# Performance work log

Measured on AMD Instinct MI355X. Metric: run time of the kernel, lower is better.

Reference implementation:

```python
import jax, jax.numpy as jnp
import numpy as np

N_NODES = 2048
N_FLUID = 400000
N_SOLID = 400000


def setup_inputs() -> dict:
    key = jax.random.key(0)
    k1, k2, k3 = jax.random.split(key, 3)
    nodes = jax.random.uniform(k1, (N_NODES, 3), dtype=jnp.float32)
    # sorted distinct node ids per tet: sort 4 draws from [0, N-4) then add offsets 0..3
    fe = jnp.sort(jax.random.randint(k2, (N_FLUID, 4), 0, N_NODES - 4), axis=1) + jnp.arange(4)
    se = jnp.sort(jax.random.randint(k3, (N_SOLID, 4), 0, N_NODES - 4), axis=1) + jnp.arange(4)
    return {
        "nodes": nodes,
        "fluid_elements": fe.astype(jnp.int32),
        "solid_elements": se.astype(jnp.int32),
        "E_mod": jnp.float32(2.1e11),
        "nu": jnp.float32(0.3),
        "rho_s": jnp.float32(7850.0),
    }


def _grads_and_volume(coords):
    """coords: [E,4,3] -> shape-fn gradients [E,4,3], volume [E]."""
    ones = jnp.ones(coords.shape[:-1] + (1,), coords.dtype)
    A = jnp.concatenate([ones, coords], axis=-1)
    A_inv = jnp.linalg.inv(A)
    grads = jnp.swapaxes(A_inv[..., 1:, :], -1, -2)        # [E,4,3]
    v0 = coords[:, 1] - coords[:, 0]
    v1 = coords[:, 2] - coords[:, 0]
    v2 = coords[:, 3] - coords[:, 0]
    vol = jnp.abs(jnp.linalg.det(jnp.stack([v0, v1, v2], axis=-1))) / 6.0  # [E]
    return grads, vol


def _fluid_element_matrices(coords):
    grads, vol = _grads_and_volume(coords)
    K_e = vol[:, None, None] * jnp.einsum("eik,ejk->eij", grads, grads)      # [E,4,4]
    m_template = (2.0 * jnp.eye(4, dtype=coords.dtype) + jnp.ones((4, 4), coords.dtype)) / 10.0
    M_e = vol[:, None, None] * m_template
    return K_e, M_e


def _elasticity_D(E_mod, nu):
    coeff = E_mod / ((1.0 + nu) * (1.0 - 2.0 * nu))
    top = nu * jnp.ones((3, 3), jnp.float32) + (1.0 - 2.0 * nu) * jnp.eye(3, dtype=jnp.float32)
    D = jnp.zeros((6, 6), jnp.float32)
    D = D.at[:3, :3].set(top)
    D = D.at[3:, 3:].set(((1.0 - 2.0 * nu) / 2.0) * jnp.eye(3, dtype=jnp.float32))
    return coeff * D


def _solid_element_matrices(coords, E_mod, nu, rho_s):
    grads, vol = _grads_and_volume(coords)                 # grads [E,4,3]
    bx, by, bz = grads[..., 0], grads[..., 1], grads[..., 2]   # each [E,4]
    z = jnp.zeros_like(bx)
    # per-node 6x3 strain-displacement block -> [E,4,6,3]
    block = jnp.stack([
        jnp.stack([bx, z, z], axis=-1),
        jnp.stack([z, by, z], axis=-1),
        jnp.stack([z, z, bz], axis=-1),
        jnp.stack([by, bx, z], axis=-1),
        jnp.stack([z, bz, by], axis=-1),
        jnp.stack([bz, z, bx], axis=-1),
    ], axis=-2)
    E = coords.shape[0]
    B = jnp.transpose(block, (0, 2, 1, 3)).reshape(E, 6, 12)  # [E,6,12]
    D = _elasticity_D(E_mod, nu)                              # [6,6]
    K_e = vol[:, None, None] * jnp.einsum("eai,ab,ebj->eij", B, D, B)  # [E,12,12]
    M_e = (rho_s * vol / 4.0)[:, None, None] * jnp.eye(12, dtype=coords.dtype)
    return K_e, M_e


def reference(nodes, fluid_elements, solid_elements, E_mod, nu, rho_s):
    n = nodes.shape[0]
    # ---- fluid: local matrices + scatter-add assembly into [N,N] ----
    cf = nodes[fluid_elements]                              # [Ef,4,3]
    Kf_e, Mf_e = _fluid_element_matrices(cf)
    rows = fluid_elements[:, :, None]                       # [Ef,4,1]
    cols = fluid_elements[:, None, :]                       # [Ef,1,4]
    K_f = jnp.zeros((n, n), jnp.float32).at[rows, cols].add(Kf_e)
    M_f = jnp.zeros((n, n), jnp.float32).at[rows, cols].add(Mf_e)
    # ---- solid: 3 dof/node, assembly into [3N,3N] ----
    cs = nodes[solid_elements]                              # [Es,4,3]
    Ks_e, Ms_e = _solid_element_matrices(cs, E_mod, nu, rho_s)
    dofs = (3 * solid_elements[:, :, None] + jnp.arange(3)).reshape(solid_elements.shape[0], 12)
    K_s = jnp.zeros((3 * n, 3 * n), jnp.float32).at[dofs[:, :, None], dofs[:, None, :]].add(Ks_e)
    M_s = jnp.zeros((3 * n, 3 * n), jnp.float32).at[dofs[:, :, None], dofs[:, None, :]].add(Ms_e)
    return (K_f, M_f, K_s, M_s)
```

## Files before the change

### kernel.cpp

```cpp
#include <hip/hip_runtime.h>


#define G_PART 256

__device__ __forceinline__ float sel4(float x0, float x1, float x2, float x3, int a) {
    float r = x0;
    r = (a == 1) ? x1 : r;
    r = (a == 2) ? x2 : r;
    r = (a == 3) ? x3 : r;
    return r;
}
__device__ __forceinline__ int sel4i(int x0, int x1, int x2, int x3, int a) {
    int r = x0;
    r = (a == 1) ? x1 : r;
    r = (a == 2) ? x2 : r;
    r = (a == 3) ? x3 : r;
    return r;
}

__device__ __forceinline__ float wave_reduce(float v) {
#pragma unroll
    for (int m = 1; m < 64; m <<= 1) v += __shfl_xor(v, m, 64);
    return v;
}

__device__ __forceinline__ void tet_geom_f(const float* __restrict__ nodes,
                                           int n0, int n1, int n2, int n3_,
                                           float& gx1, float& gy1, float& gz1,
                                           float& gx2, float& gy2, float& gz2,
                                           float& gx3, float& gy3, float& gz3,
                                           float& volf)
{
    const float* q0 = nodes + 3ll * n0;
    const float* q1 = nodes + 3ll * n1;
    const float* q2 = nodes + 3ll * n2;
    const float* q3 = nodes + 3ll * n3_;
    double p0x = q0[0], p0y = q0[1], p0z = q0[2];
    double r1x = (double)q1[0] - p0x, r1y = (double)q1[1] - p0y, r1z = (double)q1[2] - p0z;
    double r2x = (double)q2[0] - p0x, r2y = (double)q2[1] - p0y, r2z = (double)q2[2] - p0z;
    double r3x = (double)q3[0] - p0x, r3y = (double)q3[1] - p0y, r3z = (double)q3[2] - p0z;
    double c23x = r2y*r3z - r2z*r3y, c23y = r2z*r3x - r2x*r3z, c23z = r2x*r3y - r2y*r3x;
    double det = r1x*c23x + r1y*c23y + r1z*c23z;
    double inv = 1.0 / det;
    double c31x = r3y*r1z - r3z*r1y, c31y = r3z*r1x - r3x*r1z, c31z = r3x*r1y - r3y*r1x;
    double c12x = r1y*r2z - r1z*r2y, c12y = r1z*r2x - r1x*r2z, c12z = r1x*r2y - r1y*r2x;
    gx1 = (float)(c23x*inv); gy1 = (float)(c23y*inv); gz1 = (float)(c23z*inv);
    gx2 = (float)(c31x*inv); gy2 = (float)(c31y*inv); gz2 = (float)(c31z*inv);
    gx3 = (float)(c12x*inv); gy3 = (float)(c12y*inv); gz3 = (float)(c12z*inv);
    volf = (float)(fabs(det) / 6.0);
}

__device__ __forceinline__ int fetch_entry(const int* __restrict__ ent,
                                           const int* __restrict__ Sb,
                                           const int* __restrict__ Qb,
                                           int chunk4, int v)
{
    int lo = 0, hi = 255;
#pragma unroll
    for (int it = 0; it < 8; ++it) {
        int mid = (lo + hi + 1) >> 1;
        bool ge = (Qb[mid] <= v);
        lo = ge ? mid : lo;
        hi = ge ? hi : mid - 1;
    }
    return ent[(size_t)lo * chunk4 + Sb[lo] + (v - Qb[lo])];
}

#define DECL_VISIT(P) \
    float P##gx0=0,P##gx1=0,P##gx2=0,P##gx3=0, P##gy0=0,P##gy1=0,P##gy2=0,P##gy3=0, \
          P##gz0=0,P##gz1=0,P##gz2=0,P##gz3=0, P##vol=0, P##ga0=0,P##ga1=0,P##ga2=0; \
    int P##a=0, P##c0=0,P##c1=0,P##c2=0,P##c3=0;

#define LOAD_VISIT(P, packed_) do { \
    int e_ = (packed_) >> 2; P##a = (packed_) & 3; \
    int4 nd_ = elems4[e_]; \
    P##c0 = nd_.x; P##c1 = nd_.y; P##c2 = nd_.z; P##c3 = nd_.w; \
    tet_geom_f(nodes, nd_.x, nd_.y, nd_.z, nd_.w, \
        P##gx1,P##gy1,P##gz1, P##gx2,P##gy2,P##gz2, P##gx3,P##gy3,P##gz3, P##vol); \
    P##gx0 = -(P##gx1+P##gx2+P##gx3); \
    P##gy0 = -(P##gy1+P##gy2+P##gy3); \
    P##gz0 = -(P##gz1+P##gz2+P##gz3); \
    P##ga0 = sel4(P##gx0,P##gx1,P##gx2,P##gx3,P##a); \
    P##ga1 = sel4(P##gy0,P##gy1,P##gy2,P##gy3,P##a); \
    P##ga2 = sel4(P##gz0,P##gz1,P##gz2,P##gz3,P##a); \
} while (0)

#define DIAG_S(P) do { \
    float lv_ = lam*P##vol, mv_ = mu*P##vol, lm_ = lv_+mv_; \
    float mgg_ = mv_*(P##ga0*P##ga0 + P##ga1*P##ga1 + P##ga2*P##ga2); \
    d00 += lm_*P##ga0*P##ga0 + mgg_; d01 += lm_*P##ga0*P##ga1;        d02 += lm_*P##ga0*P##ga2; \
    d10 += lm_*P##ga1*P##ga0;        d11 += lm_*P##ga1*P##ga1 + mgg_; d12 += lm_*P##ga1*P##ga2; \
    d20 += lm_*P##ga2*P##ga0;        d21 += lm_*P##ga2*P##ga1;        d22 += lm_*P##ga2*P##ga2 + mgg_; \
    vsum += P##vol; } while (0)

#define DIAG_F(P) do { \
    dK += P##vol*(P##ga0*P##ga0 + P##ga1*P##ga1 + P##ga2*P##ga2); \
    dM += P##vol*0.3f; } while (0)

#define PAIR_S(P, b_) do { \
    float gb0_ = sel4(P##gx0,P##gx1,P##gx2,P##gx3,b_); \
    float gb1_ = sel4(P##gy0,P##gy1,P##gy2,P##gy3,b_); \
    float gb2_ = sel4(P##gz0,P##gz1,P##gz2,P##gz3,b_); \
    col = sel4i(P##c0,P##c1,P##c2,P##c3,b_); \
    float lv_ = lam*P##vol, mv_ = mu*P##vol; \
    float la0_ = lv_*P##ga0, la1_ = lv_*P##ga1, la2_ = lv_*P##ga2; \
    float ma0_ = mv_*P##ga0, ma1_ = mv_*P##ga1, ma2_ = mv_*P##ga2; \
    float mgg_ = mv_*(P##ga0*gb0_ + P##ga1*gb1_ + P##ga2*gb2_); \
    v00 = la0_*gb0_ + ma0_*gb0_ + mgg_; v01 = la0_*gb1_ + ma1_*gb0_; v02 = la0_*gb2_ + ma2_*gb0_; \
    v10 = la1_*gb0_ + ma0_*gb1_; v11 = la1_*gb1_ + ma1_*gb1_ + mgg_; v12 = la1_*gb2_ + ma2_*gb1_; \
    v20 = la2_*gb0_ + ma0_*gb2_; v21 = la2_*gb1_ + ma1_*gb2_; v22 = la2_*gb2_ + ma2_*gb2_ + mgg_; \
} while (0)

#define PAIR_F(P, b_) do { \
    float gb0_ = sel4(P##gx0,P##gx1,P##gx2,P##gx3,b_); \
    float gb1_ = sel4(P##gy0,P##gy1,P##gy2,P##gy3,b_); \
    float gb2_ = sel4(P##gz0,P##gz1,P##gz2,P##gz3,b_); \
    col = sel4i(P##c0,P##c1,P##c2,P##c3,b_); \
    vK = P##vol*(P##ga0*gb0_ + P##ga1*gb1_ + P##ga2*gb2_); \
    vM = P##vol*0.1f; \
} while (0)

__global__ void __launch_bounds__(256)
index_build(const int4* __restrict__ fe, const int4* __restrict__ se,
            int* __restrict__ entF, int* __restrict__ entS,
            int* __restrict__ PF, int* __restrict__ PS,
            int nf, int ns, int n, int chunkF, int chunkS)
{
    extern __shared__ int h[];
    int* wsum = h + n;
    const bool solid = blockIdx.x >= G_PART;
    const int b = solid ? blockIdx.x - G_PART : blockIdx.x;
    const int4* elems = solid ? se : fe;
    const int nelem = solid ? ns : nf;
    const int chunk = solid ? chunkS : chunkF;
    int* P = (solid ? PS : PF) + (size_t)b * (n + 1);
    int* entries = (solid ? entS : entF) + (size_t)b * 4 * chunk;

    const int t = threadIdx.x;
    const int beg = b * chunk, end = min(nelem, beg + chunk);

    for (int i = t; i < n; i += 256) h[i] = 0;
    __syncthreads();
    for (int e = beg + t; e < end; e += 256) {
        int4 nd = elems[e];
        atomicAdd(&h[nd.x], 1);
        atomicAdd(&h[nd.y], 1);
        atomicAdd(&h[nd.z], 1);
        atomicAdd(&h[nd.w], 1);
    }
    __syncthreads();

    const int cs = (n + 255) / 256;
    const int base = t * cs;
    int s = 0;
    for (int k = 0; k < cs; ++k) {
        int i = base + k;
        if (i < n) s += h[i];
    }
    wsum[t] = s;
    __syncthreads();
    for (int d = 1; d < 256; d <<= 1) {
        int v = (t >= d) ? wsum[t - d] : 0;
        __syncthreads();
        wsum[t] += v;
        __syncthreads();
    }
    int run = (t == 0) ? 0 : wsum[t - 1];
    for (int k = 0; k < cs; ++k) {
        int i = base + k;
        if (i < n) { int c = h[i]; h[i] = run; P[i] = run; run += c; }
    }
    if (t == 255) P[n] = wsum[255];
    __syncthreads();

    for (int e = beg + t; e < end; e += 256) {
        int4 nd = elems[e];
        int p;
        p = atomicAdd(&h[nd.x], 1); entries[p] = e * 4 + 0;
        p = atomicAdd(&h[nd.y], 1); entries[p] = e * 4 + 1;
        p = atomicAdd(&h[nd.z], 1); entries[p] = e * 4 + 2;
        p = atomicAdd(&h[nd.w], 1); entries[p] = e * 4 + 3;
    }
}

__global__ void __launch_bounds__(512, 4)
fused_gather(const int* __restrict__ entF, const int* __restrict__ PF,
             const int* __restrict__ entS, const int* __restrict__ PS,
             const int4* __restrict__ fe, const int4* __restrict__ se,
             const float* __restrict__ nodes,
             float* __restrict__ Kf, float* __restrict__ Mf,
             float* __restrict__ Ks, float* __restrict__ Ms,
             const float* __restrict__ E_p, const float* __restrict__ nu_p,
             const float* __restrict__ rho_p, int n, int n3,
             int chunk4F, int chunk4S)
{
    extern __shared__ unsigned char smem[];
    const int tid = threadIdx.x;
    const int bid = blockIdx.x;

    if (bid < n) {
        const int r = bid;
        const int4* elems4 = se;
        float* val = (float*)smem;
        unsigned short* claim = (unsigned short*)(val + 9 * n);
        int* Sb = (int*)(claim + n);
        int* Qb = Sb + 256;
        float* dred = (float*)(Qb + 257);

        {
            float4* v = (float4*)val;
            int cnt = (9 * n) >> 2;
            for (int k = tid; k < cnt; k += 512) v[k] = make_float4(0.f,0.f,0.f,0.f);
        }
        if (tid < 256) {
            const int* Pp = PS + (size_t)tid * (n + 1) + r;
            int s0 = Pp[0], e0 = Pp[1];
            Sb[tid] = s0;
            Qb[tid] = e0 - s0;
        }
        __syncthreads();
        if (tid < 64) {
            int c0 = Qb[4*tid], c1 = Qb[4*tid+1], c2 = Qb[4*tid+2], c3 = Qb[4*tid+3];
            int s = c0 + c1 + c2 + c3;
            int x = s;
#pragma unroll
            for (int d = 1; d < 64; d <<= 1) {
                int y = __shfl_up(x, d, 64);
                if (tid >= d) x += y;
            }
            int ex = x - s;
            Qb[4*tid] = ex; Qb[4*tid+1] = ex + c0;
            Qb[4*tid+2] = ex + c0 + c1; Qb[4*tid+3] = ex + c0 + c1 + c2;
            if (tid == 63) Qb[256] = ex + s;
        }
        __syncthreads();
        const int T = Qb[256];

        float E = *E_p, nu = *nu_p, rho = *rho_p;
        float coeff = E / ((1.f + nu) * (1.f - 2.f * nu));
        float lam = coeff * nu;
        float mu  = coeff * (1.f - 2.f * nu) * 0.5f;

        float d00=0,d01=0,d02=0,d10=0,d11=0,d12=0,d20=0,d21=0,d22=0,vsum=0;
        DECL_VISIT(A_);
        DECL_VISIT(B_);

        bool pending = false, validB = false;
        int s, col = 0, nextV = tid + 1024;
        float v00=0,v01=0,v02=0,v10=0,v11=0,v12=0,v20=0,v21=0,v22=0;

        const int vi0 = tid, vi1 = tid + 512;
        if (vi0 < T) {
            int pk = fetch_entry(entS, Sb, Qb, chunk4S, vi0);
            LOAD_VISIT(A_, pk); DIAG_S(A_); s = 0;
        } else s = 6;
        if (vi1 < T) {
            int pk = fetch_entry(entS, Sb, Qb, chunk4S, vi1);
            LOAD_VISIT(B_, pk); DIAG_S(B_); validB = true;
        }

        auto advanceS = [&]() {
            while (!pending) {
                if (s >= 6 || (s >= 3 && !validB)) {
                    if (nextV >= T) return;
                    int pk = fetch_entry(entS, Sb, Qb, chunk4S, nextV);
                    LOAD_VISIT(B_, pk); DIAG_S(B_);
                    validB = true; nextV += 512; s = 3;
                }
                if (s < 3) { int t_ = s;     int b_ = t_ + (t_ >= A_a ? 1 : 0); PAIR_S(A_, b_); }
                else       { int t_ = s - 3; int b_ = t_ + (t_ >= B_a ? 1 : 0); PAIR_S(B_, b_); }
                ++s; pending = true;
            }
        };

        advanceS();
        int live = __syncthreads_count(pending ? 1 : 0);
        while (live) {
            if (pending) claim[col] = (unsigned short)tid;
            __syncthreads();
            if (pending && claim[col] == (unsigned short)tid) {
                float* p0 = val + 3 * col;
                float* p1 = p0 + n3;
                float* p2 = p1 + n3;
                p0[0]+=v00; p0[1]+=v01; p0[2]+=v02;
                p1[0]+=v10; p1[1]+=v11; p1[2]+=v12;
                p2[0]+=v20; p2[1]+=v21; p2[2]+=v22;
                pending = false;
                advanceS();
            }
            live = __syncthreads_count(pending ? 1 : 0);
        }

        d00=wave_reduce(d00); d01=wave_reduce(d01); d02=wave_reduce(d02);
        d10=wave_reduce(d10); d11=wave_reduce(d11); d12=wave_reduce(d12);
        d20=wave_reduce(d20); d21=wave_reduce(d21); d22=wave_reduce(d22);
        vsum=wave_reduce(vsum);
        if ((tid & 63) == 0) {
            int w = tid >> 6;
            dred[w*10+0]=d00; dred[w*10+1]=d01; dred[w*10+2]=d02;
            dred[w*10+3]=d10; dred[w*10+4]=d11; dred[w*10+5]=d12;
            dred[w*10+6]=d20; dred[w*10+7]=d21; dred[w*10+8]=d22;
            dred[w*10+9]=vsum;
        }
        __syncthreads();
        if (tid < 10) {
            float t_ = 0.f;
            for (int w = 0; w < 8; ++w) t_ += dred[w*10 + tid];
            dred[80 + tid] = t_;
        }
        __syncthreads();
        if (tid < 9) {
            int i = tid / 3, j = tid - 3 * i;
            val[i * n3 + 3 * r + j] += dred[80 + tid];
        }
        __syncthreads();

        int q = n3 >> 2;
        for (int k4 = tid; k4 < 3 * q; k4 += 512) {
            int i = (k4 >= q) + (k4 >= 2*q);
            int t4 = k4 - i * q;
            float4 w = ((const float4*)(val + i * n3))[t4];
            ((float4*)(Ks + (size_t)(3*r + i) * n3))[t4] = w;
        }
        float diag = rho * 0.25f * dred[89];
        for (int k4 = tid; k4 < 3 * q; k4 += 512) {
            int i = (k4 >= q) + (k4 >= 2*q);
            int t4 = k4 - i * q;
            int dcol = 3*r + i;
            int base = t4 << 2;
            float4 w;
            w.x = (base + 0 == dcol) ? diag : 0.f;
            w.y = (base + 1 == dcol) ? diag : 0.f;
            w.z = (base + 2 == dcol) ? diag : 0.f;
            w.w = (base + 3 == dcol) ? diag : 0.f;
            ((float4*)(Ms + (size_t)(3*r + i) * n3))[t4] = w;
        }
    } else {
        const int r = bid - n;
        const int4* elems4 = fe;
        float* val = (float*)smem;
        unsigned short* claim = (unsigned short*)(val + 2 * n);
        int* Sb = (int*)(claim + n);
        int* Qb = Sb + 256;
        float* dred = (float*)(Qb + 257);

        {
            float4* v = (float4*)val;
            int cnt = (2 * n) >> 2;
            for (int k = tid; k < cnt; k += 512) v[k] = make_float4(0.f,0.f,0.f,0.f);
        }
        if (tid < 256) {
            const int* Pp = PF + (size_t)tid * (n + 1) + r;
            int s0 = Pp[0], e0 = Pp[1];
            Sb[tid] = s0;
            Qb[tid] = e0 - s0;
        }
        __syncthreads();
        if (tid < 64) {
            int c0 = Qb[4*tid], c1 = Qb[4*tid+1], c2 = Qb[4*tid+2], c3 = Qb[4*tid+3];
            int s = c0 + c1 + c2 + c3;
            int x = s;
#pragma unroll
            for (int d = 1; d < 64; d <<= 1) {
                int y = __shfl_up(x, d, 64);
                if (tid >= d) x += y;
            }
            int ex = x - s;
            Qb[4*tid] = ex; Qb[4*tid+1] = ex + c0;
            Qb[4*tid+2] = ex + c0 + c1; Qb[4*tid+3] = ex + c0 + c1 + c2;
            if (tid == 63) Qb[256] = ex + s;
        }
        __syncthreads();
        const int T = Qb[256];

        float dK = 0.f, dM = 0.f;
        DECL_VISIT(A_);
        DECL_VISIT(B_);

        bool pending = false, validB = false;
        int s, col = 0, nextV = tid + 1024;
        float vK = 0.f, vM = 0.f;

        const int vi0 = tid, vi1 = tid + 512;
        if (vi0 < T) {
            int pk = fetch_entry(entF, Sb, Qb, chunk4F, vi0);
            LOAD_VISIT(A_, pk); DIAG_F(A_); s = 0;
        } else s = 6;
        if (vi1 < T) {
            int pk = fetch_entry(entF, Sb, Qb, chunk4F, vi1);
            LOAD_VISIT(B_, pk); DIAG_F(B_); validB = true;
        }

        auto advanceF = [&]() {
            while (!pending) {
                if (s >= 6 || (s >= 3 && !validB)) {
                    if (nextV >= T) return;
                    int pk = fetch_entry(entF, Sb, Qb, chunk4F, nextV);
                    LOAD_VISIT(B_, pk); DIAG_F(B_);
                    validB = true; nextV += 512; s = 3;
                }
                if (s < 3) { int t_ = s;     int b_ = t_ + (t_ >= A_a ? 1 : 0); PAIR_F(A_, b_); }
                else       { int t_ = s - 3; int b_ = t_ + (t_ >= B_a ? 1 : 0); PAIR_F(B_, b_); }
                ++s; pending = true;
            }
        };

        advanceF();
        int live = __syncthreads_count(pending ? 1 : 0);
        while (live) {
            if (pending) claim[col] = (unsigned short)tid;
            __syncthreads();
            if (pending && claim[col] == (unsigned short)tid) {
                val[col]     += vK;
                val[n + col] += vM;
                pending = false;
                advanceF();
            }
            live = __syncthreads_count(pending ? 1 : 0);
        }

        dK = wave_reduce(dK);
        dM = wave_reduce(dM);
        if ((tid & 63) == 0) { int w = tid >> 6; dred[w*2+0] = dK; dred[w*2+1] = dM; }
        __syncthreads();
        if (tid < 2) {
            float t_ = 0.f;
            for (int w = 0; w < 8; ++w) t_ += dred[w*2 + tid];
            dred[16 + tid] = t_;
        }
        __syncthreads();
        if (tid == 0) { val[r] += dred[16]; val[n + r] += dred[17]; }
        __syncthreads();

        size_t rowoff = (size_t)r * n;
        int qf = n >> 2;
        float4* K4 = (float4*)(Kf + rowoff);
        float4* M4 = (float4*)(Mf + rowoff);
        for (int c4 = tid; c4 < qf; c4 += 512) {
            K4[c4] = ((const float4*)val)[c4];
            M4[c4] = ((const float4*)(val + n))[c4];
        }
    }
}

__device__ __forceinline__ void tet_grads_d(const float* __restrict__ nodes,
                                            const int* ni, double g[4][3], double& vol)
{
    double p[4][3];
#pragma unroll
    for (int a = 0; a < 4; ++a) {
        const float* q = nodes + 3ll * ni[a];
        p[a][0] = (double)q[0]; p[a][1] = (double)q[1]; p[a][2] = (double)q[2];
    }
    double r1[3], r2[3], r3[3];
#pragma unroll
    for (int k = 0; k < 3; ++k) {
        r1[k] = p[1][k] - p[0][k];
        r2[k] = p[2][k] - p[0][k];
        r3[k] = p[3][k] - p[0][k];
    }
    double c23[3] = { r2[1]*r3[2]-r2[2]*r3[1], r2[2]*r3[0]-r2[0]*r3[2], r2[0]*r3[1]-r2[1]*r3[0] };
    double det = r1[0]*c23[0] + r1[1]*c23[1] + r1[2]*c23[2];
    double inv = 1.0 / det;
    double c31[3] = { r3[1]*r1[2]-r3[2]*r1[1], r3[2]*r1[0]-r3[0]*r1[2], r3[0]*r1[1]-r3[1]*r1[0] };
    double c12[3] = { r1[1]*r2[2]-r1[2]*r2[1], r1[2]*r2[0]-r1[0]*r2[2], r1[0]*r2[1]-r1[1]*r2[0] };
#pragma unroll
    for (int k = 0; k < 3; ++k) {
        g[1][k] = c23[k]*inv; g[2][k] = c31[k]*inv; g[3][k] = c12[k]*inv;
        g[0][k] = -(g[1][k] + g[2][k] + g[3][k]);
    }
    vol = fabs(det) / 6.0;
}

__global__ void __launch_bounds__(256)
fluid_assemble(const float* __restrict__ nodes, const int* __restrict__ elems,
               float* __restrict__ Kf, float* __restrict__ Mf, int nelem, int n)
{
    int e = blockIdx.x * blockDim.x + threadIdx.x;
    if (e >= nelem) return;
    const int4 nd = *reinterpret_cast<const int4*>(elems + 4ll * e);
    int ni[4] = { nd.x, nd.y, nd.z, nd.w };
    double g[4][3], vol;
    tet_grads_d(nodes, ni, g, vol);
#pragma unroll
    for (int a = 0; a < 4; ++a) {
        long long rowoff = (long long)ni[a] * n;
#pragma unroll
        for (int b = 0; b < 4; ++b) {
            double kv = vol * (g[a][0]*g[b][0] + g[a][1]*g[b][1] + g[a][2]*g[b][2]);
            double mv = vol * (a == b ? 0.3 : 0.1);
            atomicAdd(Kf + rowoff + ni[b], (float)kv);
            atomicAdd(Mf + rowoff + ni[b], (float)mv);
        }
    }
}

__global__ void __launch_bounds__(256)
solid_assemble(const float* __restrict__ nodes, const int* __restrict__ elems,
               float* __restrict__ Ks, float* __restrict__ Ms,
               const float* __restrict__ E_p, const float* __restrict__ nu_p,
               const float* __restrict__ rho_p, int nelem, int n3)
{
    int e = blockIdx.x * blockDim.x + threadIdx.x;
    if (e >= nelem) return;
    double E = (double)*E_p, nu = (double)*nu_p, rho = (double)*rho_p;
    double coeff = E / ((1.0 + nu) * (1.0 - 2.0 * nu));
    double lam = coeff * nu, mu = coeff * (1.0 - 2.0 * nu) * 0.5;
    const int4 nd = *reinterpret_cast<const int4*>(elems + 4ll * e);
    int ni[4] = { nd.x, nd.y, nd.z, nd.w };
    double g[4][3], vol;
    tet_grads_d(nodes, ni, g, vol);
    double lv = lam * vol, mv = mu * vol;
#pragma unroll
    for (int a = 0; a < 4; ++a) {
        long long row0 = 3ll * ni[a];
#pragma unroll
        for (int b = 0; b < 4; ++b) {
            long long col0 = 3ll * ni[b];
            double gg = g[a][0]*g[b][0] + g[a][1]*g[b][1] + g[a][2]*g[b][2];
#pragma unroll
            for (int i = 0; i < 3; ++i) {
                float* rowp = Ks + (row0 + i) * (long long)n3 + col0;
#pragma unroll
                for (int j = 0; j < 3; ++j) {
                    double val = lv * g[a][i] * g[b][j] + mv * g[a][j] * g[b][i];
                    if (i == j) val += mv * gg;
                    atomicAdd(rowp + j, (float)val);
                }
            }
        }
        float mval = (float)(rho * vol * 0.25);
#pragma unroll
        for (int i = 0; i < 3; ++i) {
            long long d = row0 + i;
            atomicAdd(Ms + d * (long long)n3 + d, mval);
        }
    }
}

extern "C" void kernel_launch(void* const* d_in, const int* in_sizes, int n_in,
                              void* d_out, int out_size, void* d_ws, size_t ws_size,
                              hipStream_t stream)
{
    const float* nodes = (const float*)d_in[0];
    const int*   fe    = (const int*)d_in[1];
    const int*   se    = (const int*)d_in[2];
    const float* E_p   = (const float*)d_in[3];
    const float* nu_p  = (const float*)d_in[4];
    const float* rho_p = (const float*)d_in[5];

    const int n  = in_sizes[0] / 3;
    const int nf = in_sizes[1] / 4;
    const int ns = in_sizes[2] / 4;
    const int n3 = 3 * n;

    float* out = (float*)d_out;
    float* Kf = out;
    float* Mf = Kf + (size_t)n * n;
    float* Ks = Mf + (size_t)n * n;
    float* Ms = Ks + (size_t)n3 * n3;

    const int chunkF = (nf + G_PART - 1) / G_PART;
    const int chunkS = (ns + G_PART - 1) / G_PART;

    size_t pos = 0;
    auto take = [&](size_t bytes) {
        size_t p = pos;
        pos = (pos + bytes + 255) & ~(size_t)255;
        return p;
    };
    size_t entF_o = take((size_t)4 * chunkF * G_PART * 4);
    size_t entS_o = take((size_t)4 * chunkS * G_PART * 4);
    size_t PF_o   = take((size_t)G_PART * (n + 1) * 4);
    size_t PS_o   = take((size_t)G_PART * (n + 1) * 4);

    size_t gatherLds = (size_t)9 * n * 4 + (size_t)n * 2 + (256 + 257) * 4 + 96 * 4;
    size_t indexLds  = (size_t)(n + 256) * 4;
    bool gather_ok = (pos <= ws_size) && ((n & 3) == 0) && (n <= 65535) &&
                     (gatherLds <= 160 * 1024) && (indexLds <= 64 * 1024);

    const int bs = 256;

    if (!gather_ok) {
        hipMemsetAsync(d_out, 0, (size_t)out_size * sizeof(float), stream);
        fluid_assemble<<<(nf + bs - 1) / bs, bs, 0, stream>>>(nodes, fe, Kf, Mf, nf, n);
        solid_assemble<<<(ns + bs - 1) / bs, bs, 0, stream>>>(nodes, se, Ks, Ms,
                                                              E_p, nu_p, rho_p, ns, n3);
        return;
    }

    char* ws = (char*)d_ws;
    int* entF = (int*)(ws + entF_o);
    int* entS = (int*)(ws + entS_o);
    int* PF   = (int*)(ws + PF_o);
    int* PS   = (int*)(ws + PS_o);

    const int4* fe4 = (const int4*)fe;
    const int4* se4 = (const int4*)se;

    index_build<<<2 * G_PART, bs, indexLds, stream>>>(fe4, se4, entF, entS, PF, PS,
                                                      nf, ns, n, chunkF, chunkS);
    fused_gather<<<2 * n, 512, gatherLds, stream>>>(entF, PF, entS, PS,
                                                    fe4, se4, nodes,
                                                    Kf, Mf, Ks, Ms,
                                                    E_p, nu_p, rho_p, n, n3,
                                                    4 * chunkF, 4 * chunkS);
}
```

Before: 199.6 us.

## Batch per-visit column claims into lock-step rounds and transpose partition offsets

Replaces the one-pending-write-per-thread claim loop with a round-based scheme. Each thread claims all three remaining columns of both loaded visits at once, then applies every claim it wins. This cuts the number of block-wide barriers per row. The partition prefix array is transposed so per-row offset loads are coalesced. The initial visits look up their partition through an LDS table instead of binary search. Fluid and solid blocks are interleaved by block index, and the LDS limit check is tightened, which changes occupancy and shifts more inputs to the fallback path.

```diff
diff --git a/kernel.cpp b/kernel.cpp
--- a/kernel.cpp
+++ b/kernel.cpp
@@ -50,10 +50,10 @@
     volf = (float)(fabs(det) / 6.0);
 }
 
-__device__ __forceinline__ int fetch_entry(const int* __restrict__ ent,
-                                           const int* __restrict__ Sb,
-                                           const int* __restrict__ Qb,
-                                           int chunk4, int v)
+__device__ __forceinline__ int fetch_entry_bs(const int* __restrict__ ent,
+                                              const int* __restrict__ Sb,
+                                              const int* __restrict__ Qb,
+                                              int chunk4, int v)
 {
     int lo = 0, hi = 255;
 #pragma unroll
@@ -69,12 +69,11 @@
 #define DECL_VISIT(P) \
     float P##gx0=0,P##gx1=0,P##gx2=0,P##gx3=0, P##gy0=0,P##gy1=0,P##gy2=0,P##gy3=0, \
           P##gz0=0,P##gz1=0,P##gz2=0,P##gz3=0, P##vol=0, P##ga0=0,P##ga1=0,P##ga2=0; \
-    int P##a=0, P##c0=0,P##c1=0,P##c2=0,P##c3=0;
+    int P##a=0, P##k0=0, P##k1=0, P##k2=0;
 
 #define LOAD_VISIT(P, packed_) do { \
     int e_ = (packed_) >> 2; P##a = (packed_) & 3; \
     int4 nd_ = elems4[e_]; \
-    P##c0 = nd_.x; P##c1 = nd_.y; P##c2 = nd_.z; P##c3 = nd_.w; \
     tet_geom_f(nodes, nd_.x, nd_.y, nd_.z, nd_.w, \
         P##gx1,P##gy1,P##gz1, P##gx2,P##gy2,P##gz2, P##gx3,P##gy3,P##gz3, P##vol); \
     P##gx0 = -(P##gx1+P##gx2+P##gx3); \
@@ -83,6 +82,9 @@
     P##ga0 = sel4(P##gx0,P##gx1,P##gx2,P##gx3,P##a); \
     P##ga1 = sel4(P##gy0,P##gy1,P##gy2,P##gy3,P##a); \
     P##ga2 = sel4(P##gz0,P##gz1,P##gz2,P##gz3,P##a); \
+    P##k0 = sel4i(nd_.x, nd_.y, nd_.z, nd_.w, 0 + ((0 >= P##a) ? 1 : 0)); \
+    P##k1 = sel4i(nd_.x, nd_.y, nd_.z, nd_.w, 1 + ((1 >= P##a) ? 1 : 0)); \
+    P##k2 = sel4i(nd_.x, nd_.y, nd_.z, nd_.w, 2 + ((2 >= P##a) ? 1 : 0)); \
 } while (0)
 
 #define DIAG_S(P) do { \
@@ -97,28 +99,39 @@
     dK += P##vol*(P##ga0*P##ga0 + P##ga1*P##ga1 + P##ga2*P##ga2); \
     dM += P##vol*0.3f; } while (0)
 
-#define PAIR_S(P, b_) do { \
-    float gb0_ = sel4(P##gx0,P##gx1,P##gx2,P##gx3,b_); \
-    float gb1_ = sel4(P##gy0,P##gy1,P##gy2,P##gy3,b_); \
-    float gb2_ = sel4(P##gz0,P##gz1,P##gz2,P##gz3,b_); \
-    col = sel4i(P##c0,P##c1,P##c2,P##c3,b_); \
-    float lv_ = lam*P##vol, mv_ = mu*P##vol; \
-    float la0_ = lv_*P##ga0, la1_ = lv_*P##ga1, la2_ = lv_*P##ga2; \
-    float ma0_ = mv_*P##ga0, ma1_ = mv_*P##ga1, ma2_ = mv_*P##ga2; \
-    float mgg_ = mv_*(P##ga0*gb0_ + P##ga1*gb1_ + P##ga2*gb2_); \
-    v00 = la0_*gb0_ + ma0_*gb0_ + mgg_; v01 = la0_*gb1_ + ma1_*gb0_; v02 = la0_*gb2_ + ma2_*gb0_; \
-    v10 = la1_*gb0_ + ma0_*gb1_; v11 = la1_*gb1_ + ma1_*gb1_ + mgg_; v12 = la1_*gb2_ + ma2_*gb1_; \
-    v20 = la2_*gb0_ + ma0_*gb2_; v21 = la2_*gb1_ + ma1_*gb2_; v22 = la2_*gb2_ + ma2_*gb2_ + mgg_; \
-} while (0)
-
-#define PAIR_F(P, b_) do { \
-    float gb0_ = sel4(P##gx0,P##gx1,P##gx2,P##gx3,b_); \
-    float gb1_ = sel4(P##gy0,P##gy1,P##gy2,P##gy3,b_); \
-    float gb2_ = sel4(P##gz0,P##gz1,P##gz2,P##gz3,b_); \
-    col = sel4i(P##c0,P##c1,P##c2,P##c3,b_); \
-    vK = P##vol*(P##ga0*gb0_ + P##ga1*gb1_ + P##ga2*gb2_); \
-    vM = P##vol*0.1f; \
-} while (0)
+#define WIN_S(P, K, BIT) \
+    if ((slots & (BIT)) && claim[P##k##K] == (unsigned short)tid) { \
+        int b_ = (K) + (((K) >= P##a) ? 1 : 0); \
+        float gb0_ = sel4(P##gx0,P##gx1,P##gx2,P##gx3,b_); \
+        float gb1_ = sel4(P##gy0,P##gy1,P##gy2,P##gy3,b_); \
+        float gb2_ = sel4(P##gz0,P##gz1,P##gz2,P##gz3,b_); \
+        float lv_ = lam*P##vol, mv_ = mu*P##vol; \
+        float la0_=lv_*P##ga0, la1_=lv_*P##ga1, la2_=lv_*P##ga2; \
+        float ma0_=mv_*P##ga0, ma1_=mv_*P##ga1, ma2_=mv_*P##ga2; \
+        float mgg_ = mv_*(P##ga0*gb0_ + P##ga1*gb1_ + P##ga2*gb2_); \
+        float* p0_ = val + 3*P##k##K; float* p1_ = p0_ + n3; float* p2_ = p1_ + n3; \
+        p0_[0] += la0_*gb0_ + ma0_*gb0_ + mgg_; \
+        p0_[1] += la0_*gb1_ + ma1_*gb0_; \
+        p0_[2] += la0_*gb2_ + ma2_*gb0_; \
+        p1_[0] += la1_*gb0_ + ma0_*gb1_; \
+        p1_[1] += la1_*gb1_ + ma1_*gb1_ + mgg_; \
+        p1_[2] += la1_*gb2_ + ma2_*gb1_; \
+        p2_[0] += la2_*gb0_ + ma0_*gb2_; \
+        p2_[1] += la2_*gb1_ + ma1_*gb2_; \
+        p2_[2] += la2_*gb2_ + ma2_*gb2_ + mgg_; \
+        slots &= ~(BIT); \
+    }
+
+#define WIN_F(P, K, BIT) \
+    if ((slots & (BIT)) && claim[P##k##K] == (unsigned short)tid) { \
+        int b_ = (K) + (((K) >= P##a) ? 1 : 0); \
+        float gb0_ = sel4(P##gx0,P##gx1,P##gx2,P##gx3,b_); \
+        float gb1_ = sel4(P##gy0,P##gy1,P##gy2,P##gy3,b_); \
+        float gb2_ = sel4(P##gz0,P##gz1,P##gz2,P##gz3,b_); \
+        val[P##k##K]     += P##vol*(P##ga0*gb0_ + P##ga1*gb1_ + P##ga2*gb2_); \
+        val[n + P##k##K] += P##vol*0.1f; \
+        slots &= ~(BIT); \
+    }
 
 __global__ void __launch_bounds__(256)
 index_build(const int4* __restrict__ fe, const int4* __restrict__ se,
@@ -133,7 +146,7 @@
     const int4* elems = solid ? se : fe;
     const int nelem = solid ? ns : nf;
     const int chunk = solid ? chunkS : chunkF;
-    int* P = (solid ? PS : PF) + (size_t)b * (n + 1);
+    int* P2 = solid ? PS : PF;
     int* entries = (solid ? entS : entF) + (size_t)b * 4 * chunk;
 
     const int t = threadIdx.x;
@@ -168,9 +181,13 @@
     int run = (t == 0) ? 0 : wsum[t - 1];
     for (int k = 0; k < cs; ++k) {
         int i = base + k;
-        if (i < n) { int c = h[i]; h[i] = run; P[i] = run; run += c; }
-    }
-    if (t == 255) P[n] = wsum[255];
+        if (i < n) {
+            int c = h[i]; h[i] = run;
+            P2[(size_t)i * G_PART + b] = run;
+            run += c;
+        }
+    }
+    if (t == 255) P2[(size_t)n * G_PART + b] = wsum[255];
     __syncthreads();
 
     for (int e = beg + t; e < end; e += 256) {
@@ -197,15 +214,17 @@
     extern __shared__ unsigned char smem[];
     const int tid = threadIdx.x;
     const int bid = blockIdx.x;
-
-    if (bid < n) {
-        const int r = bid;
+    const bool isSolid = (bid & 1) == 0;
+    const int r = bid >> 1;
+
+    if (isSolid) {
         const int4* elems4 = se;
         float* val = (float*)smem;
         unsigned short* claim = (unsigned short*)(val + 9 * n);
         int* Sb = (int*)(claim + n);
         int* Qb = Sb + 256;
         float* dred = (float*)(Qb + 257);
+        int* flg = (int*)(dred + 90);
 
         {
             float4* v = (float4*)val;
@@ -213,11 +232,12 @@
             for (int k = tid; k < cnt; k += 512) v[k] = make_float4(0.f,0.f,0.f,0.f);
         }
         if (tid < 256) {
-            const int* Pp = PS + (size_t)tid * (n + 1) + r;
-            int s0 = Pp[0], e0 = Pp[1];
+            int s0 = PS[(size_t)r * G_PART + tid];
+            int e0 = PS[(size_t)(r + 1) * G_PART + tid];
             Sb[tid] = s0;
             Qb[tid] = e0 - s0;
         }
+        if (tid == 0) { flg[0] = 0; flg[1] = 0; }
         __syncthreads();
         if (tid < 64) {
             int c0 = Qb[4*tid], c1 = Qb[4*tid+1], c2 = Qb[4*tid+2], c3 = Qb[4*tid+3];
@@ -235,6 +255,13 @@
         }
         __syncthreads();
         const int T = Qb[256];
+        const int pvLim = min(T, n);
+
+        if (tid < 256) {
+            int v0 = Qb[tid], v1 = min(Qb[tid + 1], pvLim);
+            for (int v = v0; v < v1; ++v) claim[v] = (unsigned short)tid;
+        }
+        __syncthreads();
 
         float E = *E_p, nu = *nu_p, rho = *rho_p;
         float coeff = E / ((1.f + nu) * (1.f - 2.f * nu));
@@ -245,50 +272,49 @@
         DECL_VISIT(A_);
         DECL_VISIT(B_);
 
-        bool pending = false, validB = false;
-        int s, col = 0, nextV = tid + 1024;
-        float v00=0,v01=0,v02=0,v10=0,v11=0,v12=0,v20=0,v21=0,v22=0;
-
+        int slots = 0, nextV = tid + 1024;
         const int vi0 = tid, vi1 = tid + 512;
         if (vi0 < T) {
-            int pk = fetch_entry(entS, Sb, Qb, chunk4S, vi0);
-            LOAD_VISIT(A_, pk); DIAG_S(A_); s = 0;
-        } else s = 6;
+            int part = (vi0 < pvLim) ? (int)claim[vi0] : -1;
+            int pk = (part >= 0)
+                   ? entS[(size_t)part * chunk4S + Sb[part] + (vi0 - Qb[part])]
+                   : fetch_entry_bs(entS, Sb, Qb, chunk4S, vi0);
+            LOAD_VISIT(A_, pk); DIAG_S(A_); slots |= 0x07;
+        }
         if (vi1 < T) {
-            int pk = fetch_entry(entS, Sb, Qb, chunk4S, vi1);
-            LOAD_VISIT(B_, pk); DIAG_S(B_); validB = true;
-        }
-
-        auto advanceS = [&]() {
-            while (!pending) {
-                if (s >= 6 || (s >= 3 && !validB)) {
-                    if (nextV >= T) return;
-                    int pk = fetch_entry(entS, Sb, Qb, chunk4S, nextV);
-                    LOAD_VISIT(B_, pk); DIAG_S(B_);
-                    validB = true; nextV += 512; s = 3;
-                }
-                if (s < 3) { int t_ = s;     int b_ = t_ + (t_ >= A_a ? 1 : 0); PAIR_S(A_, b_); }
-                else       { int t_ = s - 3; int b_ = t_ + (t_ >= B_a ? 1 : 0); PAIR_S(B_, b_); }
-                ++s; pending = true;
+            int part = (vi1 < pvLim) ? (int)claim[vi1] : -1;
+            int pk = (part >= 0)
+                   ? entS[(size_t)part * chunk4S + Sb[part] + (vi1 - Qb[part])]
+                   : fetch_entry_bs(entS, Sb, Qb, chunk4S, vi1);
+            LOAD_VISIT(B_, pk); DIAG_S(B_); slots |= 0x38;
+        }
+        __syncthreads();
+
+        int p = 0;
+        for (;;) {
+            if (slots || nextV < T) flg[p] = 1;
+            if (slots & 0x01) claim[A_k0] = (unsigned short)tid;
+            if (slots & 0x02) claim[A_k1] = (unsigned short)tid;
+            if (slots & 0x04) claim[A_k2] = (unsigned short)tid;
+            if (slots & 0x08) claim[B_k0] = (unsigned short)tid;
+            if (slots & 0x10) claim[B_k1] = (unsigned short)tid;
+            if (slots & 0x20) claim[B_k2] = (unsigned short)tid;
+            __syncthreads();
+            if (!flg[p]) break;
+            if (tid == 0) flg[p ^ 1] = 0;
+            WIN_S(A_, 0, 0x01)
+            WIN_S(A_, 1, 0x02)
+            WIN_S(A_, 2, 0x04)
+            WIN_S(B_, 0, 0x08)
+            WIN_S(B_, 1, 0x10)
+            WIN_S(B_, 2, 0x20)
+            if (!slots && nextV < T) {
+                int pk = fetch_entry_bs(entS, Sb, Qb, chunk4S, nextV);
+                LOAD_VISIT(B_, pk); DIAG_S(B_);
+                slots = 0x38; nextV += 512;
             }
-        };
-
-        advanceS();
-        int live = __syncthreads_count(pending ? 1 : 0);
-        while (live) {
-            if (pending) claim[col] = (unsigned short)tid;
+            p ^= 1;
             __syncthreads();
-            if (pending && claim[col] == (unsigned short)tid) {
-                float* p0 = val + 3 * col;
-                float* p1 = p0 + n3;
-                float* p2 = p1 + n3;
-                p0[0]+=v00; p0[1]+=v01; p0[2]+=v02;
-                p1[0]+=v10; p1[1]+=v11; p1[2]+=v12;
-                p2[0]+=v20; p2[1]+=v21; p2[2]+=v22;
-                pending = false;
-                advanceS();
-            }
-            live = __syncthreads_count(pending ? 1 : 0);
         }
 
         d00=wave_reduce(d00); d01=wave_reduce(d01); d02=wave_reduce(d02);
@@ -336,13 +362,13 @@
             ((float4*)(Ms + (size_t)(3*r + i) * n3))[t4] = w;
         }
     } else {
-        const int r = bid - n;
         const int4* elems4 = fe;
         float* val = (float*)smem;
         unsigned short* claim = (unsigned short*)(val + 2 * n);
         int* Sb = (int*)(claim + n);
         int* Qb = Sb + 256;
         float* dred = (float*)(Qb + 257);
+        int* flg = (int*)(dred + 18);
 
         {
             float4* v = (float4*)val;
@@ -350,11 +376,12 @@
             for (int k = tid; k < cnt; k += 512) v[k] = make_float4(0.f,0.f,0.f,0.f);
         }
         if (tid < 256) {
-            const int* Pp = PF + (size_t)tid * (n + 1) + r;
-            int s0 = Pp[0], e0 = Pp[1];
+            int s0 = PF[(size_t)r * G_PART + tid];
+            int e0 = PF[(size_t)(r + 1) * G_PART + tid];
             Sb[tid] = s0;
             Qb[tid] = e0 - s0;
         }
+        if (tid == 0) { flg[0] = 0; flg[1] = 0; }
         __syncthreads();
         if (tid < 64) {
             int c0 = Qb[4*tid], c1 = Qb[4*tid+1], c2 = Qb[4*tid+2], c3 = Qb[4*tid+3];
@@ -372,51 +399,61 @@
         }
         __syncthreads();
         const int T = Qb[256];
+        const int pvLim = min(T, n);
+
+        if (tid < 256) {
+            int v0 = Qb[tid], v1 = min(Qb[tid + 1], pvLim);
+            for (int v = v0; v < v1; ++v) claim[v] = (unsigned short)tid;
+        }
+        __syncthreads();
 
         float dK = 0.f, dM = 0.f;
         DECL_VISIT(A_);
         DECL_VISIT(B_);
 
-        bool pending = false, validB = false;
-        int s, col = 0, nextV = tid + 1024;
-        float vK = 0.f, vM = 0.f;
-
+        int slots = 0, nextV = tid + 1024;
         const int vi0 = tid, vi1 = tid + 512;
         if (vi0 < T) {
-            int pk = fetch_entry(entF, Sb, Qb, chunk4F, vi0);
-            LOAD_VISIT(A_, pk); DIAG_F(A_); s = 0;
-        } else s = 6;
+            int part = (vi0 < pvLim) ? (int)claim[vi0] : -1;
+            int pk = (part >= 0)
+                   ? entF[(size_t)part * chunk4F + Sb[part] + (vi0 - Qb[part])]
+                   : fetch_entry_bs(entF, Sb, Qb, chunk4F, vi0);
+            LOAD_VISIT(A_, pk); DIAG_F(A_); slots |= 0x07;
+        }
         if (vi1 < T) {
-            int pk = fetch_entry(entF, Sb, Qb, chunk4F, vi1);
-            LOAD_VISIT(B_, pk); DIAG_F(B_); validB = true;
-        }
-
-        auto advanceF = [&]() {
-            while (!pending) {
-                if (s >= 6 || (s >= 3 && !validB)) {
-                    if (nextV >= T) return;
-                    int pk = fetch_entry(entF, Sb, Qb, chunk4F, nextV);
-                    LOAD_VISIT(B_, pk); DIAG_F(B_);
-                    validB = true; nextV += 512; s = 3;
-                }
-                if (s < 3) { int t_ = s;     int b_ = t_ + (t_ >= A_a ? 1 : 0); PAIR_F(A_, b_); }
-                else       { int t_ = s - 3; int b_ = t_ + (t_ >= B_a ? 1 : 0); PAIR_F(B_, b_); }
-                ++s; pending = true;
+            int part = (vi1 < pvLim) ? (int)claim[vi1] : -1;
+            int pk = (part >= 0)
+                   ? entF[(size_t)part * chunk4F + Sb[part] + (vi1 - Qb[part])]
+                   : fetch_entry_bs(entF, Sb, Qb, chunk4F, vi1);
+            LOAD_VISIT(B_, pk); DIAG_F(B_); slots |= 0x38;
+        }
+        __syncthreads();
+
+        int p = 0;
+        for (;;) {
+            if (slots || nextV < T) flg[p] = 1;
+            if (slots & 0x01) claim[A_k0] = (unsigned short)tid;
+            if (slots & 0x02) claim[A_k1] = (unsigned short)tid;
+            if (slots & 0x04) claim[A_k2] = (unsigned short)tid;
+            if (slots & 0x08) claim[B_k0] = (unsigned short)tid;
+            if (slots & 0x10) claim[B_k1] = (unsigned short)tid;
+            if (slots & 0x20) claim[B_k2] = (unsigned short)tid;
+            __syncthreads();
+            if (!flg[p]) break;
+            if (tid == 0) flg[p ^ 1] = 0;
+            WIN_F(A_, 0, 0x01)
+            WIN_F(A_, 1, 0x02)
+            WIN_F(A_, 2, 0x04)
+            WIN_F(B_, 0, 0x08)
+            WIN_F(B_, 1, 0x10)
+            WIN_F(B_, 2, 0x20)
+            if (!slots && nextV < T) {
+                int pk = fetch_entry_bs(entF, Sb, Qb, chunk4F, nextV);
+                LOAD_VISIT(B_, pk); DIAG_F(B_);
+                slots = 0x38; nextV += 512;
             }
-        };
-
-        advanceF();
-        int live = __syncthreads_count(pending ? 1 : 0);
-        while (live) {
-            if (pending) claim[col] = (unsigned short)tid;
+            p ^= 1;
             __syncthreads();
-            if (pending && claim[col] == (unsigned short)tid) {
-                val[col]     += vK;
-                val[n + col] += vM;
-                pending = false;
-                advanceF();
-            }
-            live = __syncthreads_count(pending ? 1 : 0);
         }
 
         dK = wave_reduce(dK);
@@ -571,13 +608,13 @@
     };
     size_t entF_o = take((size_t)4 * chunkF * G_PART * 4);
     size_t entS_o = take((size_t)4 * chunkS * G_PART * 4);
-    size_t PF_o   = take((size_t)G_PART * (n + 1) * 4);
-    size_t PS_o   = take((size_t)G_PART * (n + 1) * 4);
-
-    size_t gatherLds = (size_t)9 * n * 4 + (size_t)n * 2 + (256 + 257) * 4 + 96 * 4;
+    size_t PF_o   = take((size_t)(n + 1) * G_PART * 4);
+    size_t PS_o   = take((size_t)(n + 1) * G_PART * 4);
+
+    size_t gatherLds = (size_t)9 * n * 4 + (size_t)n * 2 + (256 + 257) * 4 + 90 * 4 + 8;
     size_t indexLds  = (size_t)(n + 256) * 4;
     bool gather_ok = (pos <= ws_size) && ((n & 3) == 0) && (n <= 65535) &&
-                     (gatherLds <= 160 * 1024) && (indexLds <= 64 * 1024);
+                     (gatherLds <= 80 * 1024) && (indexLds <= 64 * 1024);
 
     const int bs = 256;
 
```

New measurement: 227.4 us. 14.0% more time.

## Store full tet node tuples in CSR entries and transpose partition offsets

Applied to the files above, without the earlier changes.

The index build now writes each entry as an int4 holding the tet's four node ids, with the local vertex index packed into the high bits of the last id. This removes the dependent load of the element array during gather. Partition offsets are stored transposed so the 256 partition starts for one row sit contiguously. The first visit of each thread finds its partition through a claim-array lookup instead of a binary search. In exchange, entry storage is four times larger, n is limited to 4095 by the bit packing, and an extra barrier is added.

```diff
diff --git a/kernel.cpp b/kernel.cpp
--- a/kernel.cpp
+++ b/kernel.cpp
@@ -50,10 +50,10 @@
     volf = (float)(fabs(det) / 6.0);
 }
 
-__device__ __forceinline__ int fetch_entry(const int* __restrict__ ent,
-                                           const int* __restrict__ Sb,
-                                           const int* __restrict__ Qb,
-                                           int chunk4, int v)
+__device__ __forceinline__ int4 fetch_entry_bs(const int4* __restrict__ ent,
+                                               const int* __restrict__ Sb,
+                                               const int* __restrict__ Qb,
+                                               int chunk4, int v)
 {
     int lo = 0, hi = 255;
 #pragma unroll
@@ -71,11 +71,10 @@
           P##gz0=0,P##gz1=0,P##gz2=0,P##gz3=0, P##vol=0, P##ga0=0,P##ga1=0,P##ga2=0; \
     int P##a=0, P##c0=0,P##c1=0,P##c2=0,P##c3=0;
 
-#define LOAD_VISIT(P, packed_) do { \
-    int e_ = (packed_) >> 2; P##a = (packed_) & 3; \
-    int4 nd_ = elems4[e_]; \
-    P##c0 = nd_.x; P##c1 = nd_.y; P##c2 = nd_.z; P##c3 = nd_.w; \
-    tet_geom_f(nodes, nd_.x, nd_.y, nd_.z, nd_.w, \
+#define LOAD_VISIT(P, en_) do { \
+    int ndw_ = (en_).w & 0xFFF; P##a = (en_).w >> 12; \
+    P##c0 = (en_).x; P##c1 = (en_).y; P##c2 = (en_).z; P##c3 = ndw_; \
+    tet_geom_f(nodes, P##c0, P##c1, P##c2, P##c3, \
         P##gx1,P##gy1,P##gz1, P##gx2,P##gy2,P##gz2, P##gx3,P##gy3,P##gz3, P##vol); \
     P##gx0 = -(P##gx1+P##gx2+P##gx3); \
     P##gy0 = -(P##gy1+P##gy2+P##gy3); \
@@ -122,7 +121,7 @@
 
 __global__ void __launch_bounds__(256)
 index_build(const int4* __restrict__ fe, const int4* __restrict__ se,
-            int* __restrict__ entF, int* __restrict__ entS,
+            int4* __restrict__ entF, int4* __restrict__ entS,
             int* __restrict__ PF, int* __restrict__ PS,
             int nf, int ns, int n, int chunkF, int chunkS)
 {
@@ -133,8 +132,8 @@
     const int4* elems = solid ? se : fe;
     const int nelem = solid ? ns : nf;
     const int chunk = solid ? chunkS : chunkF;
-    int* P = (solid ? PS : PF) + (size_t)b * (n + 1);
-    int* entries = (solid ? entS : entF) + (size_t)b * 4 * chunk;
+    int* P2 = solid ? PS : PF;
+    int4* entries = (solid ? entS : entF) + (size_t)b * 4 * chunk;
 
     const int t = threadIdx.x;
     const int beg = b * chunk, end = min(nelem, beg + chunk);
@@ -168,25 +167,28 @@
     int run = (t == 0) ? 0 : wsum[t - 1];
     for (int k = 0; k < cs; ++k) {
         int i = base + k;
-        if (i < n) { int c = h[i]; h[i] = run; P[i] = run; run += c; }
-    }
-    if (t == 255) P[n] = wsum[255];
+        if (i < n) {
+            int c = h[i]; h[i] = run;
+            P2[(size_t)i * G_PART + b] = run;
+            run += c;
+        }
+    }
+    if (t == 255) P2[(size_t)n * G_PART + b] = wsum[255];
     __syncthreads();
 
     for (int e = beg + t; e < end; e += 256) {
         int4 nd = elems[e];
         int p;
-        p = atomicAdd(&h[nd.x], 1); entries[p] = e * 4 + 0;
-        p = atomicAdd(&h[nd.y], 1); entries[p] = e * 4 + 1;
-        p = atomicAdd(&h[nd.z], 1); entries[p] = e * 4 + 2;
-        p = atomicAdd(&h[nd.w], 1); entries[p] = e * 4 + 3;
+        p = atomicAdd(&h[nd.x], 1); entries[p] = make_int4(nd.x, nd.y, nd.z, nd.w);
+        p = atomicAdd(&h[nd.y], 1); entries[p] = make_int4(nd.x, nd.y, nd.z, nd.w | (1<<12));
+        p = atomicAdd(&h[nd.z], 1); entries[p] = make_int4(nd.x, nd.y, nd.z, nd.w | (2<<12));
+        p = atomicAdd(&h[nd.w], 1); entries[p] = make_int4(nd.x, nd.y, nd.z, nd.w | (3<<12));
     }
 }
 
 __global__ void __launch_bounds__(512, 4)
-fused_gather(const int* __restrict__ entF, const int* __restrict__ PF,
-             const int* __restrict__ entS, const int* __restrict__ PS,
-             const int4* __restrict__ fe, const int4* __restrict__ se,
+fused_gather(const int4* __restrict__ entF, const int* __restrict__ PF,
+             const int4* __restrict__ entS, const int* __restrict__ PS,
              const float* __restrict__ nodes,
              float* __restrict__ Kf, float* __restrict__ Mf,
              float* __restrict__ Ks, float* __restrict__ Ms,
@@ -200,7 +202,6 @@
 
     if (bid < n) {
         const int r = bid;
-        const int4* elems4 = se;
         float* val = (float*)smem;
         unsigned short* claim = (unsigned short*)(val + 9 * n);
         int* Sb = (int*)(claim + n);
@@ -213,8 +214,8 @@
             for (int k = tid; k < cnt; k += 512) v[k] = make_float4(0.f,0.f,0.f,0.f);
         }
         if (tid < 256) {
-            const int* Pp = PS + (size_t)tid * (n + 1) + r;
-            int s0 = Pp[0], e0 = Pp[1];
+            int s0 = PS[(size_t)r * G_PART + tid];
+            int e0 = PS[(size_t)(r + 1) * G_PART + tid];
             Sb[tid] = s0;
             Qb[tid] = e0 - s0;
         }
@@ -235,6 +236,13 @@
         }
         __syncthreads();
         const int T = Qb[256];
+        const int pvLim = min(T, n);
+
+        if (tid < 256) {
+            int v0 = Qb[tid], v1 = min(Qb[tid + 1], pvLim);
+            for (int v = v0; v < v1; ++v) claim[v] = (unsigned short)tid;
+        }
+        __syncthreads();
 
         float E = *E_p, nu = *nu_p, rho = *rho_p;
         float coeff = E / ((1.f + nu) * (1.f - 2.f * nu));
@@ -251,20 +259,23 @@
 
         const int vi0 = tid, vi1 = tid + 512;
         if (vi0 < T) {
-            int pk = fetch_entry(entS, Sb, Qb, chunk4S, vi0);
-            LOAD_VISIT(A_, pk); DIAG_S(A_); s = 0;
+            int part = (int)claim[vi0];
+            int4 en = entS[(size_t)part * chunk4S + Sb[part] + (vi0 - Qb[part])];
+            LOAD_VISIT(A_, en); DIAG_S(A_); s = 0;
         } else s = 6;
         if (vi1 < T) {
-            int pk = fetch_entry(entS, Sb, Qb, chunk4S, vi1);
-            LOAD_VISIT(B_, pk); DIAG_S(B_); validB = true;
+            int4 en = (vi1 < pvLim)
+                ? entS[(size_t)claim[vi1] * chunk4S + Sb[claim[vi1]] + (vi1 - Qb[claim[vi1]])]
+                : fetch_entry_bs(entS, Sb, Qb, chunk4S, vi1);
+            LOAD_VISIT(B_, en); DIAG_S(B_); validB = true;
         }
 
         auto advanceS = [&]() {
             while (!pending) {
                 if (s >= 6 || (s >= 3 && !validB)) {
                     if (nextV >= T) return;
-                    int pk = fetch_entry(entS, Sb, Qb, chunk4S, nextV);
-                    LOAD_VISIT(B_, pk); DIAG_S(B_);
+                    int4 en = fetch_entry_bs(entS, Sb, Qb, chunk4S, nextV);
+                    LOAD_VISIT(B_, en); DIAG_S(B_);
                     validB = true; nextV += 512; s = 3;
                 }
                 if (s < 3) { int t_ = s;     int b_ = t_ + (t_ >= A_a ? 1 : 0); PAIR_S(A_, b_); }
@@ -274,6 +285,8 @@
         };
 
         advanceS();
+        __syncthreads();
+
         int live = __syncthreads_count(pending ? 1 : 0);
         while (live) {
             if (pending) claim[col] = (unsigned short)tid;
@@ -337,7 +350,6 @@
         }
     } else {
         const int r = bid - n;
-        const int4* elems4 = fe;
         float* val = (float*)smem;
         unsigned short* claim = (unsigned short*)(val + 2 * n);
         int* Sb = (int*)(claim + n);
@@ -350,8 +362,8 @@
             for (int k = tid; k < cnt; k += 512) v[k] = make_float4(0.f,0.f,0.f,0.f);
         }
         if (tid < 256) {
-            const int* Pp = PF + (size_t)tid * (n + 1) + r;
-            int s0 = Pp[0], e0 = Pp[1];
+            int s0 = PF[(size_t)r * G_PART + tid];
+            int e0 = PF[(size_t)(r + 1) * G_PART + tid];
             Sb[tid] = s0;
             Qb[tid] = e0 - s0;
         }
@@ -372,6 +384,13 @@
         }
         __syncthreads();
         const int T = Qb[256];
+        const int pvLim = min(T, n);
+
+        if (tid < 256) {
+            int v0 = Qb[tid], v1 = min(Qb[tid + 1], pvLim);
+            for (int v = v0; v < v1; ++v) claim[v] = (unsigned short)tid;
+        }
+        __syncthreads();
 
         float dK = 0.f, dM = 0.f;
         DECL_VISIT(A_);
@@ -383,20 +402,23 @@
 
         const int vi0 = tid, vi1 = tid + 512;
         if (vi0 < T) {
-            int pk = fetch_entry(entF, Sb, Qb, chunk4F, vi0);
-            LOAD_VISIT(A_, pk); DIAG_F(A_); s = 0;
+            int part = (int)claim[vi0];
+            int4 en = entF[(size_t)part * chunk4F + Sb[part] + (vi0 - Qb[part])];
+            LOAD_VISIT(A_, en); DIAG_F(A_); s = 0;
         } else s = 6;
         if (vi1 < T) {
-            int pk = fetch_entry(entF, Sb, Qb, chunk4F, vi1);
-            LOAD_VISIT(B_, pk); DIAG_F(B_); validB = true;
+            int4 en = (vi1 < pvLim)
+                ? entF[(size_t)claim[vi1] * chunk4F + Sb[claim[vi1]] + (vi1 - Qb[claim[vi1]])]
+                : fetch_entry_bs(entF, Sb, Qb, chunk4F, vi1);
+            LOAD_VISIT(B_, en); DIAG_F(B_); validB = true;
         }
 
         auto advanceF = [&]() {
             while (!pending) {
                 if (s >= 6 || (s >= 3 && !validB)) {
                     if (nextV >= T) return;
-                    int pk = fetch_entry(entF, Sb, Qb, chunk4F, nextV);
-                    LOAD_VISIT(B_, pk); DIAG_F(B_);
+                    int4 en = fetch_entry_bs(entF, Sb, Qb, chunk4F, nextV);
+                    LOAD_VISIT(B_, en); DIAG_F(B_);
                     validB = true; nextV += 512; s = 3;
                 }
                 if (s < 3) { int t_ = s;     int b_ = t_ + (t_ >= A_a ? 1 : 0); PAIR_F(A_, b_); }
@@ -406,6 +428,8 @@
         };
 
         advanceF();
+        __syncthreads();
+
         int live = __syncthreads_count(pending ? 1 : 0);
         while (live) {
             if (pending) claim[col] = (unsigned short)tid;
@@ -569,15 +593,15 @@
         pos = (pos + bytes + 255) & ~(size_t)255;
         return p;
     };
-    size_t entF_o = take((size_t)4 * chunkF * G_PART * 4);
-    size_t entS_o = take((size_t)4 * chunkS * G_PART * 4);
-    size_t PF_o   = take((size_t)G_PART * (n + 1) * 4);
-    size_t PS_o   = take((size_t)G_PART * (n + 1) * 4);
-
-    size_t gatherLds = (size_t)9 * n * 4 + (size_t)n * 2 + (256 + 257) * 4 + 96 * 4;
+    size_t entF_o = take((size_t)4 * chunkF * G_PART * 16);
+    size_t entS_o = take((size_t)4 * chunkS * G_PART * 16);
+    size_t PF_o   = take((size_t)(n + 1) * G_PART * 4);
+    size_t PS_o   = take((size_t)(n + 1) * G_PART * 4);
+
+    size_t gatherLds = (size_t)9 * n * 4 + (size_t)n * 2 + (256 + 257) * 4 + 90 * 4;
     size_t indexLds  = (size_t)(n + 256) * 4;
-    bool gather_ok = (pos <= ws_size) && ((n & 3) == 0) && (n <= 65535) &&
-                     (gatherLds <= 160 * 1024) && (indexLds <= 64 * 1024);
+    bool gather_ok = (pos <= ws_size) && ((n & 3) == 0) && (n <= 4095) &&
+                     (gatherLds <= 80 * 1024) && (indexLds <= 64 * 1024);
 
     const int bs = 256;
 
@@ -590,10 +614,10 @@
     }
 
     char* ws = (char*)d_ws;
-    int* entF = (int*)(ws + entF_o);
-    int* entS = (int*)(ws + entS_o);
-    int* PF   = (int*)(ws + PF_o);
-    int* PS   = (int*)(ws + PS_o);
+    int4* entF = (int4*)(ws + entF_o);
+    int4* entS = (int4*)(ws + entS_o);
+    int* PF    = (int*)(ws + PF_o);
+    int* PS    = (int*)(ws + PS_o);
 
     const int4* fe4 = (const int4*)fe;
     const int4* se4 = (const int4*)se;
@@ -601,7 +625,7 @@
     index_build<<<2 * G_PART, bs, indexLds, stream>>>(fe4, se4, entF, entS, PF, PS,
                                                       nf, ns, n, chunkF, chunkS);
     fused_gather<<<2 * n, 512, gatherLds, stream>>>(entF, PF, entS, PS,
-                                                    fe4, se4, nodes,
+                                                    nodes,
                                                     Kf, Mf, Ks, Ms,
                                                     E_p, nu_p, rho_p, n, n3,
                                                     4 * chunkF, 4 * chunkS);
```

Result: slower. 208.3 us (+4.4%).
